# Performance work log

Measured on AMD Instinct MI355X. Metric: run time of the kernel, lower is better.

The kernel has to match this reference:

```python
import jax, jax.numpy as jnp
import numpy as np

VOL_SHAPE = (192, 192, 192)
BATCH = 2
CHANNELS = 1


def setup_inputs() -> dict:
    key = jax.random.key(0)
    k1, k2 = jax.random.split(key)
    vol = jax.random.normal(k1, (BATCH,) + VOL_SHAPE + (CHANNELS,), dtype=jnp.float32)
    # near-identity affine (3,4) per batch element, as in rigid/affine motion correction
    eye = jnp.concatenate([jnp.eye(3, dtype=jnp.float32), jnp.zeros((3, 1), jnp.float32)], axis=1)
    affine = eye[None] + 0.02 * jax.random.normal(k2, (BATCH, 3, 4), dtype=jnp.float32)
    return {"vol": vol, "affine": affine}


def _warp(vol, affine):
    # vol: [B, D, H, W, C], affine: [B, 3, 4]
    B, D, H, W, C = vol.shape
    shape = (D, H, W)
    # --- affine_to_dense_shift (shift_center=True, ij indexing) ---
    ranges = [jnp.arange(s, dtype=jnp.float32) for s in shape]
    mesh = jnp.stack(jnp.meshgrid(*ranges, indexing='ij'), axis=-1)  # [D,H,W,3]
    center = jnp.array([(s - 1) / 2.0 for s in shape], dtype=jnp.float32)
    centered = mesh - center                                          # shifted grid
    homog = jnp.concatenate([centered, jnp.ones(shape + (1,), jnp.float32)], axis=-1)  # [D,H,W,4]
    loc_aff = jnp.einsum('bij,dhwj->bdhwi', affine, homog)            # [B,D,H,W,3]
    shift = loc_aff - centered                                        # dense warp field
    # --- SpatialTransformer: sample at grid + shift ---
    loc = mesh + shift                                                # [B,D,H,W,3]

    maxl = jnp.array([s - 1 for s in shape], dtype=jnp.float32)

    def interp_one(v, l):
        # v: [D,H,W,C], l: [D,H,W,3]; trilinear interp, clamp-to-edge (fill_value=None)
        cl = jnp.clip(l, 0.0, maxl)
        l0 = jnp.clip(jnp.floor(l), 0.0, maxl)
        l1 = jnp.clip(l0 + 1.0, 0.0, maxl)
        w_c0 = l1 - cl          # weight used with the floor corner (diff_loc1)
        w_c1 = 1.0 - w_c0       # weight used with the ceil corner  (diff_loc0)
        i0 = l0.astype(jnp.int32)
        i1 = l1.astype(jnp.int32)
        out = jnp.zeros(v.shape[:-1] + (v.shape[-1],), v.dtype)
        for c in range(8):  # 2^3 cube corners (fixed small loop)
            bits = ((c >> 2) & 1, (c >> 1) & 1, c & 1)
            idx = [(i1 if b else i0)[..., d] for d, b in enumerate(bits)]
            w = jnp.ones(l.shape[:-1], v.dtype)
            for d, b in enumerate(bits):
                w = w * (w_c1 if b else w_c0)[..., d]
            out = out + v[idx[0], idx[1], idx[2]] * w[..., None]
        return out

    return jax.vmap(interp_one)(vol, loc)


def reference(vol, affine):
    return _warp(vol, affine)
```

## Files before the change

kernel.cpp:

```cpp
#include <hip/hip_runtime.h>

#define DIM   192
#define PLANE (DIM * DIM)
#define NB    2
#define DPT   4
#define BH    4

typedef float f2 __attribute__((ext_vector_type(2), aligned(4)));

__global__ __launch_bounds__(256) __attribute__((amdgpu_waves_per_eu(4, 4))) void
SpatialTransformer_warp_kernel(const float* __restrict__ vol,
                               const float* __restrict__ affine,
                               float* __restrict__ out) {
    const int tid = threadIdx.x;
    const int w   = (blockIdx.x << 6) + (tid & 63);
    const int h   = blockIdx.y * BH + (tid >> 6);
    const int z   = blockIdx.z;
    const int b   = (z >= DIM / DPT) ? 1 : 0;
    const int d0  = (z - b * (DIM / DPT)) * DPT;

    const float* __restrict__ A = affine + b * 12;
    const float a00 = A[0], a01 = A[1], a02 = A[2],  a03 = A[3];
    const float a10 = A[4], a11 = A[5], a12 = A[6],  a13 = A[7];
    const float a20 = A[8], a21 = A[9], a22 = A[10], a23 = A[11];

    const float center = (DIM - 1) * 0.5f;
    const float maxl   = (float)(DIM - 1);
    const float maxi0  = (float)(DIM - 2);
    const float fplane = (float)PLANE;
    const float fdim   = (float)DIM;

    const float ch = (float)h - center;
    const float cw = (float)w - center;

    const float pd = a01 * ch + a02 * cw + a03 + center;
    const float ph = a11 * ch + a12 * cw + a13 + center;
    const float pw = a21 * ch + a22 * cw + a23 + center;

    const float* __restrict__ vb = vol + (size_t)b * DIM * PLANE;
    float* __restrict__ ob = out + ((size_t)b * DIM + d0) * PLANE
                                 + (size_t)h * DIM + w;

    f2 r00[DPT], r01[DPT], r10[DPT], r11[DPT];
    float w0d_[DPT], w0h_[DPT], w0w_[DPT];

#pragma unroll
    for (int k = 0; k < DPT; ++k) {
        const float cd = (float)(d0 + k) - center;
        const float ld = a00 * cd + pd;
        const float lh = a10 * cd + ph;
        const float lw = a20 * cd + pw;

        const float td = __builtin_amdgcn_fmed3f(ld, 0.0f, maxl);
        const float th = __builtin_amdgcn_fmed3f(lh, 0.0f, maxl);
        const float tw = __builtin_amdgcn_fmed3f(lw, 0.0f, maxl);

        const float fd = fminf(floorf(td), maxi0);
        const float fh = fminf(floorf(th), maxi0);
        const float fw = fminf(floorf(tw), maxi0);

        w0d_[k] = fd + 1.0f - td;
        w0h_[k] = fh + 1.0f - th;
        w0w_[k] = fw + 1.0f - tw;

        const int idx = (int)__builtin_fmaf(fd, fplane, __builtin_fmaf(fh, fdim, fw));
        const float* p = vb + idx;

        r00[k] = *(const f2*)(p);
        r01[k] = *(const f2*)(p + DIM);
        r10[k] = *(const f2*)(p + PLANE);
        r11[k] = *(const f2*)(p + PLANE + DIM);
    }

    __builtin_amdgcn_sched_barrier(0);

#pragma unroll
    for (int k = 0; k < DPT; ++k) {
        const float w0w = w0w_[k], w1w = 1.0f - w0w;
        const float w0h = w0h_[k], w1h = 1.0f - w0h;
        const float w0d = w0d_[k], w1d = 1.0f - w0d;

        const float x00 = r00[k].x * w0w + r00[k].y * w1w;
        const float x01 = r01[k].x * w0w + r01[k].y * w1w;
        const float x10 = r10[k].x * w0w + r10[k].y * w1w;
        const float x11 = r11[k].x * w0w + r11[k].y * w1w;

        const float y0 = x00 * w0h + x01 * w1h;
        const float y1 = x10 * w0h + x11 * w1h;

        __builtin_nontemporal_store(y0 * w0d + y1 * w1d, ob + k * PLANE);
    }
}

extern "C" void kernel_launch(void* const* d_in, const int* in_sizes, int n_in,
                              void* d_out, int out_size, void* d_ws, size_t ws_size,
                              hipStream_t stream) {
    const float* vol    = (const float*)d_in[0];
    const float* affine = (const float*)d_in[1];
    float* out = (float*)d_out;

    dim3 grid(DIM / 64, DIM / BH, NB * (DIM / DPT));
    dim3 block(256);
    SpatialTransformer_warp_kernel<<<grid, block, 0, stream>>>(vol, affine, out);
}
```

Baseline: 122.9 us.

## Stage per-block source halo tile in LDS for trilinear gathers

Each block cooperatively loads a clamped 12x16x80 source window, chosen from the affine-mapped block center, into shared memory with 16-byte loads. The eight corner reads then come from LDS, with a fallback to global loads when a sample falls outside the window. The block grows to 512 threads covering 8 rows. This trades scattered global gathers for coalesced tile loads, at the cost of about 60KB of LDS per block, a barrier, and redundant halo traffic that may lower occupancy.

```diff
diff --git a/kernel.cpp b/kernel.cpp
--- a/kernel.cpp
+++ b/kernel.cpp
@@ -4,16 +4,28 @@
 #define PLANE (DIM * DIM)
 #define NB    2
 #define DPT   4
-#define BH    4
+#define BH    8
+#define BW    64
+#define NTHREADS (BW * BH)
+
+#define SW 80
+#define SH 16
+#define SD 12
+#define SPLANE (SH * SW)
+#define NELEM  (SD * SH * SW)
+#define NGROUP (NELEM / 4)
 
 typedef float f2 __attribute__((ext_vector_type(2), aligned(4)));
+typedef float f4 __attribute__((ext_vector_type(4), aligned(16)));
 
-__global__ __launch_bounds__(256) __attribute__((amdgpu_waves_per_eu(4, 4))) void
+__global__ __launch_bounds__(NTHREADS) __attribute__((amdgpu_waves_per_eu(4, 4))) void
 SpatialTransformer_warp_kernel(const float* __restrict__ vol,
                                const float* __restrict__ affine,
                                float* __restrict__ out) {
+    __shared__ float lds[NELEM];
+
     const int tid = threadIdx.x;
-    const int w   = (blockIdx.x << 6) + (tid & 63);
+    const int w   = blockIdx.x * BW + (tid & 63);
     const int h   = blockIdx.y * BH + (tid >> 6);
     const int z   = blockIdx.z;
     const int b   = (z >= DIM / DPT) ? 1 : 0;
@@ -27,22 +39,53 @@
     const float center = (DIM - 1) * 0.5f;
     const float maxl   = (float)(DIM - 1);
     const float maxi0  = (float)(DIM - 2);
-    const float fplane = (float)PLANE;
-    const float fdim   = (float)DIM;
 
-    const float ch = (float)h - center;
-    const float cw = (float)w - center;
+    const float ccd = (float)d0 + (DPT - 1) * 0.5f - center;
+    const float cch = (float)(blockIdx.y * BH) + (BH - 1) * 0.5f - center;
+    const float ccw = (float)(blockIdx.x * BW) + (BW - 1) * 0.5f - center;
 
-    const float pd = a01 * ch + a02 * cw + a03 + center;
-    const float ph = a11 * ch + a12 * cw + a13 + center;
-    const float pw = a21 * ch + a22 * cw + a23 + center;
+    const float lcd = a00 * ccd + a01 * cch + a02 * ccw + a03 + center;
+    const float lch = a10 * ccd + a11 * cch + a12 * ccw + a13 + center;
+    const float lcw = a20 * ccd + a21 * cch + a22 * ccw + a23 + center;
+
+    const int od = (int)floorf(lcd) - (SD / 2 - 1);
+    const int oh = (int)floorf(lch) - (SH / 2 - 1);
+    const int ow = ((int)floorf(lcw) - 38) & ~3;
 
     const float* __restrict__ vb = vol + (size_t)b * DIM * PLANE;
+
+#pragma unroll
+    for (int i = 0; i < 8; ++i) {
+        const int g = i * NTHREADS + tid;
+        if (g < NGROUP) {
+            const int rw4 = (g % (SW / 4)) << 2;
+            const int t   = g / (SW / 4);
+            const int rh  = t % SH;
+            const int rd  = t / SH;
+            int cd = od + rd; cd = cd < 0 ? 0 : (cd > DIM - 1 ? DIM - 1 : cd);
+            int ch = oh + rh; ch = ch < 0 ? 0 : (ch > DIM - 1 ? DIM - 1 : ch);
+            const int gw = ow + rw4;
+            const float* rowp = vb + cd * PLANE + ch * DIM;
+            f4 v;
+            if ((unsigned)gw <= (unsigned)(DIM - 4)) {
+                v = *(const f4*)(rowp + gw);
+            } else {
+                const float s = rowp[gw < 0 ? 0 : DIM - 1];
+                v = (f4){s, s, s, s};
+            }
+            *(f4*)(&lds[g << 2]) = v;
+        }
+    }
+    __syncthreads();
+
+    const float chh = (float)h - center;
+    const float cww = (float)w - center;
+    const float pd = a01 * chh + a02 * cww + a03 + center;
+    const float ph = a11 * chh + a12 * cww + a13 + center;
+    const float pw = a21 * chh + a22 * cww + a23 + center;
+
     float* __restrict__ ob = out + ((size_t)b * DIM + d0) * PLANE
                                  + (size_t)h * DIM + w;
-
-    f2 r00[DPT], r01[DPT], r10[DPT], r11[DPT];
-    float w0d_[DPT], w0h_[DPT], w0w_[DPT];
 
 #pragma unroll
     for (int k = 0; k < DPT; ++k) {
@@ -59,31 +102,42 @@
         const float fh = fminf(floorf(th), maxi0);
         const float fw = fminf(floorf(tw), maxi0);
 
-        w0d_[k] = fd + 1.0f - td;
-        w0h_[k] = fh + 1.0f - th;
-        w0w_[k] = fw + 1.0f - tw;
+        const float w0d = fd + 1.0f - td;
+        const float w0h = fh + 1.0f - th;
+        const float w0w = fw + 1.0f - tw;
 
-        const int idx = (int)__builtin_fmaf(fd, fplane, __builtin_fmaf(fh, fdim, fw));
-        const float* p = vb + idx;
+        const int ifd = (int)fd, ifh = (int)fh, ifw = (int)fw;
+        const int rd = ifd - od, rh = ifh - oh, rw = ifw - ow;
 
-        r00[k] = *(const f2*)(p);
-        r01[k] = *(const f2*)(p + DIM);
-        r10[k] = *(const f2*)(p + PLANE);
-        r11[k] = *(const f2*)(p + PLANE + DIM);
-    }
+        float v00x, v00y, v01x, v01y, v10x, v10y, v11x, v11y;
+        if ((unsigned)rd <= (unsigned)(SD - 2) &&
+            (unsigned)rh <= (unsigned)(SH - 2) &&
+            (unsigned)rw <= (unsigned)(SW - 2)) {
+            const float* p = &lds[rd * SPLANE + rh * SW + rw];
+            v00x = p[0];           v00y = p[1];
+            v01x = p[SW];          v01y = p[SW + 1];
+            v10x = p[SPLANE];      v10y = p[SPLANE + 1];
+            v11x = p[SPLANE + SW]; v11y = p[SPLANE + SW + 1];
+        } else {
+            const float* p = vb + (ifd * PLANE + ifh * DIM + ifw);
+            const f2 r00 = *(const f2*)(p);
+            const f2 r01 = *(const f2*)(p + DIM);
+            const f2 r10 = *(const f2*)(p + PLANE);
+            const f2 r11 = *(const f2*)(p + PLANE + DIM);
+            v00x = r00.x; v00y = r00.y;
+            v01x = r01.x; v01y = r01.y;
+            v10x = r10.x; v10y = r10.y;
+            v11x = r11.x; v11y = r11.y;
+        }
 
-    __builtin_amdgcn_sched_barrier(0);
+        const float w1w = 1.0f - w0w;
+        const float w1h = 1.0f - w0h;
+        const float w1d = 1.0f - w0d;
 
-#pragma unroll
-    for (int k = 0; k < DPT; ++k) {
-        const float w0w = w0w_[k], w1w = 1.0f - w0w;
-        const float w0h = w0h_[k], w1h = 1.0f - w0h;
-        const float w0d = w0d_[k], w1d = 1.0f - w0d;
-
-        const float x00 = r00[k].x * w0w + r00[k].y * w1w;
-        const float x01 = r01[k].x * w0w + r01[k].y * w1w;
-        const float x10 = r10[k].x * w0w + r10[k].y * w1w;
-        const float x11 = r11[k].x * w0w + r11[k].y * w1w;
+        const float x00 = v00x * w0w + v00y * w1w;
+        const float x01 = v01x * w0w + v01y * w1w;
+        const float x10 = v10x * w0w + v10y * w1w;
+        const float x11 = v11x * w0w + v11y * w1w;
 
         const float y0 = x00 * w0h + x01 * w1h;
         const float y1 = x10 * w0h + x11 * w1h;
@@ -99,7 +153,7 @@
     const float* affine = (const float*)d_in[1];
     float* out = (float*)d_out;
 
-    dim3 grid(DIM / 64, DIM / BH, NB * (DIM / DPT));
-    dim3 block(256);
+    dim3 grid(DIM / BW, DIM / BH, NB * (DIM / DPT));
+    dim3 block(NTHREADS);
     SpatialTransformer_warp_kernel<<<grid, block, 0, stream>>>(vol, affine, out);
 }
```

New measurement: 173.9 us. 1.42x slower.

## Compute two adjacent outputs per thread sharing one 4-wide gather

Applied to the files above, without the earlier changes.

Each thread now produces two neighbouring W outputs. It loads 4-wide rows once and reuses them for the second voxel when both fall in the same depth/height cell, and falls back to a separate 2-wide gather otherwise. The block shape changes to 96x4 threads with a 2D grid, and stores become 2-wide. The aim is to cut redundant global loads and per-voxel index math. The cost is extra select logic, a possibly divergent fallback path, the removal of the load/compute scheduling barrier, and a changed occupancy hint.

```diff
diff --git a/kernel.cpp b/kernel.cpp
--- a/kernel.cpp
+++ b/kernel.cpp
@@ -7,17 +7,18 @@
 #define BH    4
 
 typedef float f2 __attribute__((ext_vector_type(2), aligned(4)));
+typedef float f4 __attribute__((ext_vector_type(4), aligned(4)));
 
-__global__ __launch_bounds__(256) __attribute__((amdgpu_waves_per_eu(4, 4))) void
+__global__ __launch_bounds__(96 * BH) __attribute__((amdgpu_waves_per_eu(3, 8))) void
 SpatialTransformer_warp_kernel(const float* __restrict__ vol,
                                const float* __restrict__ affine,
                                float* __restrict__ out) {
-    const int tid = threadIdx.x;
-    const int w   = (blockIdx.x << 6) + (tid & 63);
-    const int h   = blockIdx.y * BH + (tid >> 6);
-    const int z   = blockIdx.z;
-    const int b   = (z >= DIM / DPT) ? 1 : 0;
-    const int d0  = (z - b * (DIM / DPT)) * DPT;
+    const int q  = threadIdx.x;
+    const int h  = blockIdx.x * BH + threadIdx.y;
+    const int z  = blockIdx.y;
+    const int b  = (z >= DIM / DPT) ? 1 : 0;
+    const int d0 = (z - b * (DIM / DPT)) * DPT;
+    const int w0 = q << 1;
 
     const float* __restrict__ A = affine + b * 12;
     const float a00 = A[0], a01 = A[1], a02 = A[2],  a03 = A[3];
@@ -30,65 +31,98 @@
     const float fplane = (float)PLANE;
     const float fdim   = (float)DIM;
 
-    const float ch = (float)h - center;
-    const float cw = (float)w - center;
+    const float ch  = (float)h  - center;
+    const float cw0 = (float)w0 - center;
 
-    const float pd = a01 * ch + a02 * cw + a03 + center;
-    const float ph = a11 * ch + a12 * cw + a13 + center;
-    const float pw = a21 * ch + a22 * cw + a23 + center;
+    const float pd0 = a01 * ch + a02 * cw0 + a03 + center;
+    const float ph0 = a11 * ch + a12 * cw0 + a13 + center;
+    const float pw0 = a21 * ch + a22 * cw0 + a23 + center;
+    const float pd1 = pd0 + a02;
+    const float ph1 = ph0 + a12;
+    const float pw1 = pw0 + a22;
 
     const float* __restrict__ vb = vol + (size_t)b * DIM * PLANE;
     float* __restrict__ ob = out + ((size_t)b * DIM + d0) * PLANE
-                                 + (size_t)h * DIM + w;
-
-    f2 r00[DPT], r01[DPT], r10[DPT], r11[DPT];
-    float w0d_[DPT], w0h_[DPT], w0w_[DPT];
+                                 + (size_t)h * DIM + w0;
 
 #pragma unroll
     for (int k = 0; k < DPT; ++k) {
         const float cd = (float)(d0 + k) - center;
-        const float ld = a00 * cd + pd;
-        const float lh = a10 * cd + ph;
-        const float lw = a20 * cd + pw;
 
-        const float td = __builtin_amdgcn_fmed3f(ld, 0.0f, maxl);
-        const float th = __builtin_amdgcn_fmed3f(lh, 0.0f, maxl);
-        const float tw = __builtin_amdgcn_fmed3f(lw, 0.0f, maxl);
+        const float td0 = __builtin_amdgcn_fmed3f(__builtin_fmaf(a00, cd, pd0), 0.0f, maxl);
+        const float th0 = __builtin_amdgcn_fmed3f(__builtin_fmaf(a10, cd, ph0), 0.0f, maxl);
+        const float tw0 = __builtin_amdgcn_fmed3f(__builtin_fmaf(a20, cd, pw0), 0.0f, maxl);
+        const float td1 = __builtin_amdgcn_fmed3f(__builtin_fmaf(a00, cd, pd1), 0.0f, maxl);
+        const float th1 = __builtin_amdgcn_fmed3f(__builtin_fmaf(a10, cd, ph1), 0.0f, maxl);
+        const float tw1 = __builtin_amdgcn_fmed3f(__builtin_fmaf(a20, cd, pw1), 0.0f, maxl);
 
-        const float fd = fminf(floorf(td), maxi0);
-        const float fh = fminf(floorf(th), maxi0);
-        const float fw = fminf(floorf(tw), maxi0);
+        const float fd0  = fminf(floorf(td0), maxi0);
+        const float fh0  = fminf(floorf(th0), maxi0);
+        const float fw0c = fminf(floorf(tw0), maxi0);
+        const float fd1  = fminf(floorf(td1), maxi0);
+        const float fh1  = fminf(floorf(th1), maxi0);
+        const float fw1c = fminf(floorf(tw1), maxi0);
 
-        w0d_[k] = fd + 1.0f - td;
-        w0h_[k] = fh + 1.0f - th;
-        w0w_[k] = fw + 1.0f - tw;
+        const float fbw = fminf(fw0c, (float)(DIM - 4));
+        const int base = (int)__builtin_fmaf(fd0, fplane, __builtin_fmaf(fh0, fdim, fbw));
+        const float* p = vb + base;
 
-        const int idx = (int)__builtin_fmaf(fd, fplane, __builtin_fmaf(fh, fdim, fw));
-        const float* p = vb + idx;
+        const f4 vA = *(const f4*)(p);
+        const f4 vB = *(const f4*)(p + DIM);
+        const f4 vC = *(const f4*)(p + PLANE);
+        const f4 vD = *(const f4*)(p + PLANE + DIM);
 
-        r00[k] = *(const f2*)(p);
-        r01[k] = *(const f2*)(p + DIM);
-        r10[k] = *(const f2*)(p + PLANE);
-        r11[k] = *(const f2*)(p + PLANE + DIM);
-    }
+        const float fo0 = fw0c - fbw;
+        float A0x = vA.x, A0y = vA.y, B0x = vB.x, B0y = vB.y;
+        float C0x = vC.x, C0y = vC.y, D0x = vD.x, D0y = vD.y;
+        if (__any(fo0 != 0.0f)) {
+            const bool g1 = (fo0 == 1.0f), g2 = (fo0 == 2.0f);
+            A0x = g2 ? vA.z : (g1 ? vA.y : vA.x);  A0y = g2 ? vA.w : (g1 ? vA.z : vA.y);
+            B0x = g2 ? vB.z : (g1 ? vB.y : vB.x);  B0y = g2 ? vB.w : (g1 ? vB.z : vB.y);
+            C0x = g2 ? vC.z : (g1 ? vC.y : vC.x);  C0y = g2 ? vC.w : (g1 ? vC.z : vC.y);
+            D0x = g2 ? vD.z : (g1 ? vD.y : vD.x);  D0y = g2 ? vD.w : (g1 ? vD.z : vD.y);
+        }
 
-    __builtin_amdgcn_sched_barrier(0);
+        const float fo1 = fw1c - fbw;
+        const bool share = (fd1 == fd0) & (fh1 == fh0) & (fo1 >= 0.0f) & (fo1 <= 2.0f);
+        float A1x, A1y, B1x, B1y, C1x, C1y, D1x, D1y;
+        if (share) {
+            const bool e1 = (fo1 == 1.0f), e2 = (fo1 == 2.0f);
+            A1x = e2 ? vA.z : (e1 ? vA.y : vA.x);  A1y = e2 ? vA.w : (e1 ? vA.z : vA.y);
+            B1x = e2 ? vB.z : (e1 ? vB.y : vB.x);  B1y = e2 ? vB.w : (e1 ? vB.z : vB.y);
+            C1x = e2 ? vC.z : (e1 ? vC.y : vC.x);  C1y = e2 ? vC.w : (e1 ? vC.z : vC.y);
+            D1x = e2 ? vD.z : (e1 ? vD.y : vD.x);  D1y = e2 ? vD.w : (e1 ? vD.z : vD.y);
+        } else {
+            const int i1 = (int)__builtin_fmaf(fd1, fplane, __builtin_fmaf(fh1, fdim, fw1c));
+            const float* p1 = vb + i1;
+            const f2 tA = *(const f2*)(p1);
+            const f2 tB = *(const f2*)(p1 + DIM);
+            const f2 tC = *(const f2*)(p1 + PLANE);
+            const f2 tD = *(const f2*)(p1 + PLANE + DIM);
+            A1x = tA.x; A1y = tA.y;  B1x = tB.x; B1y = tB.y;
+            C1x = tC.x; C1y = tC.y;  D1x = tD.x; D1y = tD.y;
+        }
 
-#pragma unroll
-    for (int k = 0; k < DPT; ++k) {
-        const float w0w = w0w_[k], w1w = 1.0f - w0w;
-        const float w0h = w0h_[k], w1h = 1.0f - w0h;
-        const float w0d = w0d_[k], w1d = 1.0f - w0d;
+        const float u0 = fw0c + 1.0f - tw0, u1 = 1.0f - u0;
+        const float v0 = fh0  + 1.0f - th0, v1 = 1.0f - v0;
+        const float s0 = fd0  + 1.0f - td0, s1 = 1.0f - s0;
+        const float U0 = fw1c + 1.0f - tw1, U1 = 1.0f - U0;
+        const float V0 = fh1  + 1.0f - th1, V1 = 1.0f - V0;
+        const float S0 = fd1  + 1.0f - td1, S1 = 1.0f - S0;
 
-        const float x00 = r00[k].x * w0w + r00[k].y * w1w;
-        const float x01 = r01[k].x * w0w + r01[k].y * w1w;
-        const float x10 = r10[k].x * w0w + r10[k].y * w1w;
-        const float x11 = r11[k].x * w0w + r11[k].y * w1w;
+        const float x00 = A0x * u0 + A0y * u1;
+        const float x01 = B0x * u0 + B0y * u1;
+        const float x10 = C0x * u0 + C0y * u1;
+        const float x11 = D0x * u0 + D0y * u1;
+        const float r0 = (x00 * v0 + x01 * v1) * s0 + (x10 * v0 + x11 * v1) * s1;
 
-        const float y0 = x00 * w0h + x01 * w1h;
-        const float y1 = x10 * w0h + x11 * w1h;
+        const float X00 = A1x * U0 + A1y * U1;
+        const float X01 = B1x * U0 + B1y * U1;
+        const float X10 = C1x * U0 + C1y * U1;
+        const float X11 = D1x * U0 + D1y * U1;
+        const float r1 = (X00 * V0 + X01 * V1) * S0 + (X10 * V0 + X11 * V1) * S1;
 
-        __builtin_nontemporal_store(y0 * w0d + y1 * w1d, ob + k * PLANE);
+        __builtin_nontemporal_store((f2){r0, r1}, (f2*)(ob + k * PLANE));
     }
 }
 
@@ -99,7 +133,7 @@
     const float* affine = (const float*)d_in[1];
     float* out = (float*)d_out;
 
-    dim3 grid(DIM / 64, DIM / BH, NB * (DIM / DPT));
-    dim3 block(256);
+    dim3 grid(DIM / BH, NB * (DIM / DPT));
+    dim3 block(96, BH);
     SpatialTransformer_warp_kernel<<<grid, block, 0, stream>>>(vol, affine, out);
 }
```

Result: slower. 127.8 us (+4.0%).

## Enlarge per-thread depth loop and block size, drop explicit load batching

Applied to the files above, without the earlier changes.

Each thread now walks 32 depth slices in a loop unrolled by 4, instead of 4 fully batched slices. Blocks grow to 64x8 threads, and the waves-per-EU pin and sched_barrier that batched all loads before the math are removed. The aim is to cut block count and launch overhead and to reuse the per-thread setup over more outputs. The cost is fewer blocks, which may hurt latency hiding and load balance, and compiler-chosen load scheduling in place of the explicit batching.

```diff
diff --git a/kernel.cpp b/kernel.cpp
--- a/kernel.cpp
+++ b/kernel.cpp
@@ -3,21 +3,23 @@
 #define DIM   192
 #define PLANE (DIM * DIM)
 #define NB    2
-#define DPT   4
-#define BH    4
+#define BW    64
+#define BH    8
+#define BD    32
+#define NDT   (DIM / BD)
 
 typedef float f2 __attribute__((ext_vector_type(2), aligned(4)));
 
-__global__ __launch_bounds__(256) __attribute__((amdgpu_waves_per_eu(4, 4))) void
+__global__ __launch_bounds__(BW * BH) void
 SpatialTransformer_warp_kernel(const float* __restrict__ vol,
                                const float* __restrict__ affine,
                                float* __restrict__ out) {
     const int tid = threadIdx.x;
-    const int w   = (blockIdx.x << 6) + (tid & 63);
+    const int w   = blockIdx.x * BW + (tid & 63);
     const int h   = blockIdx.y * BH + (tid >> 6);
     const int z   = blockIdx.z;
-    const int b   = (z >= DIM / DPT) ? 1 : 0;
-    const int d0  = (z - b * (DIM / DPT)) * DPT;
+    const int b   = (z >= NDT) ? 1 : 0;
+    const int d0  = (z - b * NDT) * BD;
 
     const float* __restrict__ A = affine + b * 12;
     const float a00 = A[0], a01 = A[1], a02 = A[2],  a03 = A[3];
@@ -41,15 +43,12 @@
     float* __restrict__ ob = out + ((size_t)b * DIM + d0) * PLANE
                                  + (size_t)h * DIM + w;
 
-    f2 r00[DPT], r01[DPT], r10[DPT], r11[DPT];
-    float w0d_[DPT], w0h_[DPT], w0w_[DPT];
-
-#pragma unroll
-    for (int k = 0; k < DPT; ++k) {
+#pragma unroll 4
+    for (int k = 0; k < BD; ++k) {
         const float cd = (float)(d0 + k) - center;
-        const float ld = a00 * cd + pd;
-        const float lh = a10 * cd + ph;
-        const float lw = a20 * cd + pw;
+        const float ld = __builtin_fmaf(a00, cd, pd);
+        const float lh = __builtin_fmaf(a10, cd, ph);
+        const float lw = __builtin_fmaf(a20, cd, pw);
 
         const float td = __builtin_amdgcn_fmed3f(ld, 0.0f, maxl);
         const float th = __builtin_amdgcn_fmed3f(lh, 0.0f, maxl);
@@ -59,31 +58,26 @@
         const float fh = fminf(floorf(th), maxi0);
         const float fw = fminf(floorf(tw), maxi0);
 
-        w0d_[k] = fd + 1.0f - td;
-        w0h_[k] = fh + 1.0f - th;
-        w0w_[k] = fw + 1.0f - tw;
+        const float w0d = fd + 1.0f - td;
+        const float w0h = fh + 1.0f - th;
+        const float w0w = fw + 1.0f - tw;
 
         const int idx = (int)__builtin_fmaf(fd, fplane, __builtin_fmaf(fh, fdim, fw));
         const float* p = vb + idx;
 
-        r00[k] = *(const f2*)(p);
-        r01[k] = *(const f2*)(p + DIM);
-        r10[k] = *(const f2*)(p + PLANE);
-        r11[k] = *(const f2*)(p + PLANE + DIM);
-    }
+        const f2 r00 = *(const f2*)(p);
+        const f2 r01 = *(const f2*)(p + DIM);
+        const f2 r10 = *(const f2*)(p + PLANE);
+        const f2 r11 = *(const f2*)(p + PLANE + DIM);
 
-    __builtin_amdgcn_sched_barrier(0);
+        const float w1w = 1.0f - w0w;
+        const float w1h = 1.0f - w0h;
+        const float w1d = 1.0f - w0d;
 
-#pragma unroll
-    for (int k = 0; k < DPT; ++k) {
-        const float w0w = w0w_[k], w1w = 1.0f - w0w;
-        const float w0h = w0h_[k], w1h = 1.0f - w0h;
-        const float w0d = w0d_[k], w1d = 1.0f - w0d;
-
-        const float x00 = r00[k].x * w0w + r00[k].y * w1w;
-        const float x01 = r01[k].x * w0w + r01[k].y * w1w;
-        const float x10 = r10[k].x * w0w + r10[k].y * w1w;
-        const float x11 = r11[k].x * w0w + r11[k].y * w1w;
+        const float x00 = r00.x * w0w + r00.y * w1w;
+        const float x01 = r01.x * w0w + r01.y * w1w;
+        const float x10 = r10.x * w0w + r10.y * w1w;
+        const float x11 = r11.x * w0w + r11.y * w1w;
 
         const float y0 = x00 * w0h + x01 * w1h;
         const float y1 = x10 * w0h + x11 * w1h;
@@ -99,7 +93,7 @@
     const float* affine = (const float*)d_in[1];
     float* out = (float*)d_out;
 
-    dim3 grid(DIM / 64, DIM / BH, NB * (DIM / DPT));
-    dim3 block(256);
+    dim3 grid(DIM / BW, DIM / BH, NB * NDT);
+    dim3 block(BW * BH);
     SpatialTransformer_warp_kernel<<<grid, block, 0, stream>>>(vol, affine, out);
 }
```

New measurement: 142.8 us. 1.16x slower.
